# Optimization experiments

Measured on AMD Instinct MI355X. Metric: run time of the kernel, lower is better.

The kernel has to match this reference:

```python
import jax, jax.numpy as jnp
import numpy as np

HEADS = 16
D_MODEL = 1024
D_HEAD = D_MODEL // HEADS


def setup_inputs() -> dict:
    key = jax.random.key(0)
    ks = jax.random.split(key, 9)
    s_h = 1.0 / np.sqrt(D_HEAD)
    s_m = 1.0 / np.sqrt(D_MODEL)
    return {
        "x": jax.random.normal(ks[0], (4, 2048, D_MODEL), dtype=jnp.float32),
        "Wq": jax.random.uniform(ks[1], (D_HEAD, D_HEAD), jnp.float32, -s_h, s_h),
        "bq": jax.random.uniform(ks[2], (D_HEAD,), jnp.float32, -s_h, s_h),
        "Wk": jax.random.uniform(ks[3], (D_HEAD, D_HEAD), jnp.float32, -s_h, s_h),
        "bk": jax.random.uniform(ks[4], (D_HEAD,), jnp.float32, -s_h, s_h),
        "Wv": jax.random.uniform(ks[5], (D_HEAD, D_HEAD), jnp.float32, -s_h, s_h),
        "bv": jax.random.uniform(ks[6], (D_HEAD,), jnp.float32, -s_h, s_h),
        "Wp": jax.random.uniform(ks[7], (D_MODEL, D_MODEL), jnp.float32, -s_m, s_m),
        "bp": jax.random.uniform(ks[8], (D_MODEL,), jnp.float32, -s_m, s_m),
    }


def reference(x, Wq, bq, Wk, bk, Wv, bv, Wp, bp):
    B, T, C = x.shape
    xh = x.reshape(B, T, HEADS, D_HEAD)  # [B,T,H,Dh]
    # per-head linear projections (torch Linear: x @ W.T + b)
    q = jnp.einsum('bthd,ed->bhte', xh, Wq) + bq  # [B,H,T,Dh]
    k = jnp.einsum('bthd,ed->bhte', xh, Wk) + bk
    v = jnp.einsum('bthd,ed->bhte', xh, Wv) + bv
    # NOTE: original scales by sqrt(C) = sqrt(d_model), not sqrt(d_head)
    att = jnp.einsum('bhqd,bhkd->bhqk', q, k) / jnp.sqrt(jnp.float32(C))
    att = jax.nn.softmax(att, axis=-1)
    out = jnp.einsum('bhqk,bhkd->bhqd', att, v)  # [B,H,T,Dh]
    out = out.transpose(0, 2, 1, 3).reshape(B, T, C)
    return out @ Wp.T + bp
```

## Files before the change

### kernel.cpp

```cpp
#include <hip/hip_runtime.h>
#include <hip/hip_bf16.h>
#include <cstddef>

#define B_  4
#define T_  2048
#define H_  16
#define DH  64
#define C_  1024
#define BH  64

typedef float  f32x16 __attribute__((ext_vector_type(16)));
typedef __bf16 bf16x8 __attribute__((ext_vector_type(8)));
typedef __bf16 bf16x4 __attribute__((ext_vector_type(4)));

#define MFMA32(a, b, c) __builtin_amdgcn_mfma_f32_32x32x16_bf16(a, b, c, 0, 0, 0)


__device__ __forceinline__ unsigned cvt_pk_bf16(float lo, float hi) {
    unsigned r;
    asm("v_cvt_pk_bf16_f32 %0, %1, %2" : "=v"(r) : "v"(lo), "v"(hi));
    return r;
}

__global__ __launch_bounds__(256) void qkv_kernel(
    const float* __restrict__ x,
    const float* __restrict__ Wq, const float* __restrict__ bq,
    const float* __restrict__ Wk, const float* __restrict__ bk,
    const float* __restrict__ Wv, const float* __restrict__ bv,
    __bf16* __restrict__ q, __bf16* __restrict__ k, __bf16* __restrict__ vt)
{
    __shared__ __bf16 Xs[128 * 72];
    __shared__ __bf16 Ws[3][64 * 72];
    __bf16* Vtl = Xs;

    const int tt  = blockIdx.x;
    const int bh  = blockIdx.y;
    const int b   = bh >> 4, h = bh & 15;
    const int t0  = tt * 128;
    const int tid = threadIdx.x;
    const int wave = tid >> 6, lane = tid & 63;
    const int m = lane & 31, hh = lane >> 5;

    #pragma unroll
    for (int i = 0; i < 8; ++i) {
        const int idx = i * 256 + tid;
        const int r = idx >> 4, c = (idx & 15) * 4;
        const float4 x4 = *(const float4*)(x + ((size_t)(b * T_ + t0 + r)) * C_ + h * DH + c);
        const unsigned lo = ((unsigned)__builtin_bit_cast(unsigned short, (__bf16)x4.y) << 16)
                          | (unsigned)__builtin_bit_cast(unsigned short, (__bf16)x4.x);
        const unsigned hi = ((unsigned)__builtin_bit_cast(unsigned short, (__bf16)x4.w) << 16)
                          | (unsigned)__builtin_bit_cast(unsigned short, (__bf16)x4.z);
        *(unsigned*)&Xs[r * 72 + c]     = lo;
        *(unsigned*)&Xs[r * 72 + c + 2] = hi;
    }
    #pragma unroll
    for (int i = 0; i < 4; ++i) {
        const int idx = i * 256 + tid;
        const int r = idx >> 4, c = (idx & 15) * 4;
        const float* wsrc[3] = {Wq, Wk, Wv};
        #pragma unroll
        for (int wv_ = 0; wv_ < 3; ++wv_) {
            const float4 w4 = *(const float4*)(wsrc[wv_] + r * 64 + c);
            const unsigned lo = ((unsigned)__builtin_bit_cast(unsigned short, (__bf16)w4.y) << 16)
                              | (unsigned)__builtin_bit_cast(unsigned short, (__bf16)w4.x);
            const unsigned hi = ((unsigned)__builtin_bit_cast(unsigned short, (__bf16)w4.w) << 16)
                              | (unsigned)__builtin_bit_cast(unsigned short, (__bf16)w4.z);
            *(unsigned*)&Ws[wv_][r * 72 + c]     = lo;
            *(unsigned*)&Ws[wv_][r * 72 + c + 2] = hi;
        }
    }
    __syncthreads();

    bf16x8 xf[4];
    #pragma unroll
    for (int ks = 0; ks < 4; ++ks)
        xf[ks] = *(const bf16x8*)&Xs[(wave * 32 + m) * 72 + ks * 16 + hh * 8];
    __syncthreads();

    const float s32 = 0.03125f * 1.4426950408889634f;

    #pragma unroll
    for (int mat = 0; mat < 3; ++mat) {
        f32x16 acc0 = {}, acc1 = {};
        #pragma unroll
        for (int ks = 0; ks < 4; ++ks) {
            const bf16x8 w0 = *(const bf16x8*)&Ws[mat][(m) * 72 + ks * 16 + hh * 8];
            const bf16x8 w1 = *(const bf16x8*)&Ws[mat][(32 + m) * 72 + ks * 16 + hh * 8];
            acc0 = MFMA32(xf[ks], w0, acc0);
            acc1 = MFMA32(xf[ks], w1, acc1);
        }
        const float* bias = (mat == 0) ? bq : (mat == 1) ? bk : bv;
        const float b0 = bias[m], b1 = bias[32 + m];
        #pragma unroll
        for (int r = 0; r < 16; ++r) {
            const int R = (r & 3) + 8 * (r >> 2) + 4 * hh;
            const int tloc = wave * 32 + R;
            const float v0 = acc0[r] + b0, v1 = acc1[r] + b1;
            if (mat == 0) {
                const size_t base = ((size_t)bh * T_ + t0 + tloc) * DH;
                q[base + m]      = (__bf16)(v0 * s32);
                q[base + 32 + m] = (__bf16)(v1 * s32);
            } else if (mat == 1) {
                const size_t base = ((size_t)bh * T_ + t0 + tloc) * DH;
                k[base + m]      = (__bf16)v0;
                k[base + 32 + m] = (__bf16)v1;
            } else {
                Vtl[(m) * 136 + tloc]      = (__bf16)v0;
                Vtl[(32 + m) * 136 + tloc] = (__bf16)v1;
            }
        }
    }
    __syncthreads();
    #pragma unroll
    for (int i = 0; i < 4; ++i) {
        const int idx = i * 256 + tid;
        const int e = idx >> 4, c = (idx & 15) * 8;
        *(uint4*)(vt + ((size_t)(bh * 64 + e)) * T_ + t0 + c) = *(uint4*)&Vtl[e * 136 + c];
    }
}

__global__ __launch_bounds__(256, 2) void attn_kernel(
    const __bf16* __restrict__ q, const __bf16* __restrict__ k,
    const __bf16* __restrict__ vt, __bf16* __restrict__ o)
{
    __shared__ __bf16 smem[2][2][64 * 72];

    const int bh  = blockIdx.x;
    const int q0  = blockIdx.y * 256;
    const int tid = threadIdx.x;
    const int wave = tid >> 6, lane = tid & 63;
    const int m = lane & 31, h = lane >> 5;

    const __bf16* qb = q  + (size_t)bh * T_ * DH;
    const __bf16* kb = k  + (size_t)bh * T_ * DH;
    const __bf16* vb = vt + (size_t)bh * DH * T_;

    bf16x8 qf[2][4];
    #pragma unroll
    for (int hf = 0; hf < 2; ++hf)
        #pragma unroll
        for (int ks = 0; ks < 4; ++ks)
            qf[hf][ks] = *(const bf16x8*)(qb +
                (size_t)(q0 + wave * 64 + hf * 32 + m) * DH + ks * 16 + h * 8);

    const int r0s = tid >> 3;
    const int c0s = (tid & 7) * 8;

    uint4 kreg[2], vreg[2];
    #pragma unroll
    for (int i = 0; i < 2; ++i) {
        kreg[i] = *(const uint4*)(kb + (size_t)(r0s + 32 * i) * DH + c0s);
        vreg[i] = *(const uint4*)(vb + (size_t)(r0s + 32 * i) * T_ + c0s);
    }
    #pragma unroll
    for (int i = 0; i < 2; ++i) {
        *(uint4*)&smem[0][0][(r0s + 32 * i) * 72 + c0s] = kreg[i];
        *(uint4*)&smem[0][1][(r0s + 32 * i) * 72 + c0s] = vreg[i];
    }

    f32x16 O00 = {}, O01 = {}, O10 = {}, O11 = {};
    float ls0 = 0.f, ls1 = 0.f;

    int cur = 0;
    for (int kt = 0; kt < T_; kt += 64) {
        __syncthreads();
        const bool pre = (kt + 64 < T_);
        if (pre) {
            #pragma unroll
            for (int i = 0; i < 2; ++i) {
                kreg[i] = *(const uint4*)(kb + (size_t)(kt + 64 + r0s + 32 * i) * DH + c0s);
                vreg[i] = *(const uint4*)(vb + (size_t)(r0s + 32 * i) * T_ + kt + 64 + c0s);
            }
        }
        const __bf16* Ksb  = &smem[cur][0][0];
        const __bf16* Vtsb = &smem[cur][1][0];

        bf16x8 kf[2][4], vf[2][4];
        #pragma unroll
        for (int rh = 0; rh < 2; ++rh)
            #pragma unroll
            for (int ks = 0; ks < 4; ++ks)
                kf[rh][ks] = *(const bf16x8*)&Ksb[(rh * 32 + m) * 72 + ks * 16 + h * 8];
        #pragma unroll
        for (int dh = 0; dh < 2; ++dh)
            #pragma unroll
            for (int c = 0; c < 4; ++c)
                vf[dh][c] = *(const bf16x8*)&Vtsb[(dh * 32 + m) * 72 + c * 16 + h * 8];

        #pragma unroll
        for (int hf = 0; hf < 2; ++hf) {
            float lsum = 0.f;
            #pragma unroll
            for (int rh = 0; rh < 2; ++rh) {
                f32x16 S = {};
                #pragma unroll
                for (int ks = 0; ks < 4; ++ks)
                    S = MFMA32(kf[rh][ks], qf[hf][ks], S);

                #pragma unroll
                for (int cc = 0; cc < 2; ++cc) {
                    const int rb = cc * 8;
                    float e0 = __builtin_amdgcn_exp2f(S[rb + 0]);
                    float e1 = __builtin_amdgcn_exp2f(S[rb + 1]);
                    float e2 = __builtin_amdgcn_exp2f(S[rb + 2]);
                    float e3 = __builtin_amdgcn_exp2f(S[rb + 3]);
                    float e4 = __builtin_amdgcn_exp2f(S[rb + 4]);
                    float e5 = __builtin_amdgcn_exp2f(S[rb + 5]);
                    float e6 = __builtin_amdgcn_exp2f(S[rb + 6]);
                    float e7 = __builtin_amdgcn_exp2f(S[rb + 7]);
                    lsum += ((e0 + e1) + (e2 + e3)) + ((e4 + e5) + (e6 + e7));
                    unsigned a0 = cvt_pk_bf16(e0, e1);
                    unsigned a1 = cvt_pk_bf16(e2, e3);
                    unsigned b0 = cvt_pk_bf16(e4, e5);
                    unsigned b1 = cvt_pk_bf16(e6, e7);
                    asm("v_permlane32_swap_b32 %0, %1" : "+v"(a0), "+v"(b0));
                    asm("v_permlane32_swap_b32 %0, %1" : "+v"(a1), "+v"(b1));
                    const uint4 pw = {a0, a1, b0, b1};
                    const bf16x8 pb = __builtin_bit_cast(bf16x8, pw);
                    const int c = rh * 2 + cc;
                    if (hf == 0) {
                        O00 = MFMA32(vf[0][c], pb, O00);
                        O01 = MFMA32(vf[1][c], pb, O01);
                    } else {
                        O10 = MFMA32(vf[0][c], pb, O10);
                        O11 = MFMA32(vf[1][c], pb, O11);
                    }
                }
            }
            if (hf == 0) ls0 += lsum; else ls1 += lsum;
        }

        if (pre) {
            #pragma unroll
            for (int i = 0; i < 2; ++i) {
                *(uint4*)&smem[cur ^ 1][0][(r0s + 32 * i) * 72 + c0s] = kreg[i];
                *(uint4*)&smem[cur ^ 1][1][(r0s + 32 * i) * 72 + c0s] = vreg[i];
            }
        }
        cur ^= 1;
    }

    ls0 += __shfl_xor(ls0, 32);
    ls1 += __shfl_xor(ls1, 32);
    const float li0 = 1.0f / ls0, li1 = 1.0f / ls1;

    __syncthreads();
    __bf16* Os = &smem[0][0][0];

    #pragma unroll
    for (int g = 0; g < 4; ++g) {
        bf16x4 w00, w01, w10, w11;
        #pragma unroll
        for (int j = 0; j < 4; ++j) {
            w00[j] = (__bf16)(O00[4 * g + j] * li0);
            w01[j] = (__bf16)(O01[4 * g + j] * li0);
            w10[j] = (__bf16)(O10[4 * g + j] * li1);
            w11[j] = (__bf16)(O11[4 * g + j] * li1);
        }
        const int row0 = (wave * 64 + m) * 72;
        const int row1 = (wave * 64 + 32 + m) * 72;
        *(bf16x4*)&Os[row0 + 8 * g + 4 * h]      = w00;
        *(bf16x4*)&Os[row0 + 32 + 8 * g + 4 * h] = w01;
        *(bf16x4*)&Os[row1 + 8 * g + 4 * h]      = w10;
        *(bf16x4*)&Os[row1 + 32 + 8 * g + 4 * h] = w11;
    }
    __syncthreads();

    __bf16* ob = o + ((size_t)bh * T_ + q0) * DH;
    #pragma unroll
    for (int i = 0; i < 8; ++i) {
        const int idx = i * 256 + tid;
        const int r = idx >> 3, c = (idx & 7) * 8;
        *(uint4*)(ob + (size_t)r * DH + c) = *(uint4*)&Os[r * 72 + c];
    }
}

__global__ __launch_bounds__(256) void wpconv_kernel(
    const float* __restrict__ Wp, __bf16* __restrict__ Wpb)
{
    const size_t idx = (size_t)(blockIdx.x * 256 + threadIdx.x) * 4;
    const float4 w4 = *(const float4*)(Wp + idx);
    const unsigned lo = ((unsigned)__builtin_bit_cast(unsigned short, (__bf16)w4.y) << 16)
                      | (unsigned)__builtin_bit_cast(unsigned short, (__bf16)w4.x);
    const unsigned hi = ((unsigned)__builtin_bit_cast(unsigned short, (__bf16)w4.w) << 16)
                      | (unsigned)__builtin_bit_cast(unsigned short, (__bf16)w4.z);
    uint2 p; p.x = lo; p.y = hi;
    *(uint2*)(Wpb + idx) = p;
}

__global__ __launch_bounds__(256) void proj_kernel(
    const __bf16* __restrict__ a,
    const __bf16* __restrict__ Wpb, const float* __restrict__ bp,
    float* __restrict__ out)
{
    __shared__ __bf16 As[128 * 72];
    __shared__ __bf16 Bs[128 * 72];

    const int tb = blockIdx.x, eb = blockIdx.y;
    const int tid = threadIdx.x;
    const int wave = tid >> 6, lane = tid & 63;
    const int m = lane & 31, h = lane >> 5;
    const int tok0 = tb * 128;
    const int b = tok0 >> 11, t0 = tok0 & (T_ - 1);
    const int e0 = eb * 128;

    f32x16 acc[4] = {f32x16{}, f32x16{}, f32x16{}, f32x16{}};

    for (int cb = 0; cb < 16; ++cb) {
        __syncthreads();
        #pragma unroll
        for (int i = 0; i < 4; ++i) {
            const int idx = i * 256 + tid;
            const int r = idx >> 3, c = (idx & 7) * 8;
            *(uint4*)&As[r * 72 + c] =
                *(const uint4*)(a + ((size_t)(b * H_ + cb) * T_ + t0 + r) * DH + c);
        }
        #pragma unroll
        for (int i = 0; i < 4; ++i) {
            const int idx = i * 256 + tid;
            const int r = idx >> 3, c = (idx & 7) * 8;
            *(uint4*)&Bs[r * 72 + c] =
                *(const uint4*)(Wpb + (size_t)(e0 + r) * C_ + cb * 64 + c);
        }
        __syncthreads();

        #pragma unroll
        for (int ks = 0; ks < 4; ++ks) {
            const bf16x8 af = *(const bf16x8*)&As[(wave * 32 + m) * 72 + ks * 16 + h * 8];
            #pragma unroll
            for (int n = 0; n < 4; ++n) {
                const bf16x8 bf = *(const bf16x8*)&Bs[(n * 32 + m) * 72 + ks * 16 + h * 8];
                acc[n] = MFMA32(af, bf, acc[n]);
            }
        }
    }

    #pragma unroll
    for (int n = 0; n < 4; ++n) {
        const int e = e0 + n * 32 + m;
        const float bias = bp[e];
        #pragma unroll
        for (int r = 0; r < 16; ++r) {
            const int R = (r & 3) + 8 * (r >> 2) + 4 * h;
            out[(size_t)(tok0 + wave * 32 + R) * C_ + e] = acc[n][r] + bias;
        }
    }
}

extern "C" void kernel_launch(void* const* d_in, const int* in_sizes, int n_in,
                              void* d_out, int out_size, void* d_ws, size_t ws_size,
                              hipStream_t stream)
{
    const float* x  = (const float*)d_in[0];
    const float* Wq = (const float*)d_in[1];
    const float* bq = (const float*)d_in[2];
    const float* Wk = (const float*)d_in[3];
    const float* bk = (const float*)d_in[4];
    const float* Wv = (const float*)d_in[5];
    const float* bv = (const float*)d_in[6];
    const float* Wp = (const float*)d_in[7];
    const float* bp = (const float*)d_in[8];

    const size_t N = (size_t)BH * T_ * DH;
    __bf16* qws  = (__bf16*)d_ws;
    __bf16* kws  = qws + N;
    __bf16* vtws = kws + N;
    __bf16* ows  = vtws + N;
    __bf16* wpb  = qws;

    qkv_kernel<<<dim3(16, 64), 256, 0, stream>>>(
        x, Wq, bq, Wk, bk, Wv, bv, qws, kws, vtws);
    attn_kernel<<<dim3(64, 8), 256, 0, stream>>>(qws, kws, vtws, ows);
    wpconv_kernel<<<dim3(1024), 256, 0, stream>>>(Wp, wpb);
    proj_kernel<<<dim3(64, 8), 256, 0, stream>>>(ows, wpb, bp, (float*)d_out);
}
```

Baseline: 229.5 us.

## Load K/V fragments directly from global into registers, dropping LDS staging

Removes the shared-memory double buffer for K and V tiles in the attention kernel. Each wave now loads its MFMA fragments straight from global memory, prefetching the next K tile into registers through an A/B ping-pong. V fragments are loaded at the start of each tile. This eliminates the per-tile __syncthreads and the LDS store/load round trips, but each of the 4 waves now fetches the same K/V data separately, relying on L1/L2 to absorb the redundancy. The V loads are not prefetched ahead of use.

```diff
diff --git a/kernel.cpp b/kernel.cpp
--- a/kernel.cpp
+++ b/kernel.cpp
@@ -119,11 +119,75 @@
     }
 }
 
+__device__ __forceinline__ void attn_tile(
+    const __bf16* __restrict__ kb, const __bf16* __restrict__ vb,
+    int kt, int ktn,
+    const bf16x8 (&kcur)[2][4], bf16x8 (&knxt)[2][4],
+    const bf16x8 (&qf)[2][4],
+    f32x16& O00, f32x16& O01, f32x16& O10, f32x16& O11,
+    float& ls0, float& ls1, int m, int h)
+{
+    bf16x8 vf[2][4];
+    #pragma unroll
+    for (int dh = 0; dh < 2; ++dh)
+        #pragma unroll
+        for (int c = 0; c < 4; ++c)
+            vf[dh][c] = *(const bf16x8*)(vb + (size_t)(dh * 32 + m) * T_ + kt + c * 16 + h * 8);
+    #pragma unroll
+    for (int rh = 0; rh < 2; ++rh)
+        #pragma unroll
+        for (int ks = 0; ks < 4; ++ks)
+            knxt[rh][ks] = *(const bf16x8*)(kb + (size_t)(ktn + rh * 32 + m) * DH + ks * 16 + h * 8);
+
+    #pragma unroll
+    for (int hf = 0; hf < 2; ++hf) {
+        float lsum = 0.f;
+        #pragma unroll
+        for (int rh = 0; rh < 2; ++rh) {
+            f32x16 S = {};
+            #pragma unroll
+            for (int ks = 0; ks < 4; ++ks)
+                S = MFMA32(kcur[rh][ks], qf[hf][ks], S);
+
+            #pragma unroll
+            for (int cc = 0; cc < 2; ++cc) {
+                const int rb = cc * 8;
+                float e0 = __builtin_amdgcn_exp2f(S[rb + 0]);
+                float e1 = __builtin_amdgcn_exp2f(S[rb + 1]);
+                float e2 = __builtin_amdgcn_exp2f(S[rb + 2]);
+                float e3 = __builtin_amdgcn_exp2f(S[rb + 3]);
+                float e4 = __builtin_amdgcn_exp2f(S[rb + 4]);
+                float e5 = __builtin_amdgcn_exp2f(S[rb + 5]);
+                float e6 = __builtin_amdgcn_exp2f(S[rb + 6]);
+                float e7 = __builtin_amdgcn_exp2f(S[rb + 7]);
+                lsum += ((e0 + e1) + (e2 + e3)) + ((e4 + e5) + (e6 + e7));
+                unsigned a0 = cvt_pk_bf16(e0, e1);
+                unsigned a1 = cvt_pk_bf16(e2, e3);
+                unsigned b0 = cvt_pk_bf16(e4, e5);
+                unsigned b1 = cvt_pk_bf16(e6, e7);
+                asm("v_permlane32_swap_b32 %0, %1" : "+v"(a0), "+v"(b0));
+                asm("v_permlane32_swap_b32 %0, %1" : "+v"(a1), "+v"(b1));
+                const uint4 pw = {a0, a1, b0, b1};
+                const bf16x8 pb = __builtin_bit_cast(bf16x8, pw);
+                const int c = rh * 2 + cc;
+                if (hf == 0) {
+                    O00 = MFMA32(vf[0][c], pb, O00);
+                    O01 = MFMA32(vf[1][c], pb, O01);
+                } else {
+                    O10 = MFMA32(vf[0][c], pb, O10);
+                    O11 = MFMA32(vf[1][c], pb, O11);
+                }
+            }
+        }
+        if (hf == 0) ls0 += lsum; else ls1 += lsum;
+    }
+}
+
 __global__ __launch_bounds__(256, 2) void attn_kernel(
     const __bf16* __restrict__ q, const __bf16* __restrict__ k,
     const __bf16* __restrict__ vt, __bf16* __restrict__ o)
 {
-    __shared__ __bf16 smem[2][2][64 * 72];
+    __shared__ __bf16 Os[256 * 72];
 
     const int bh  = blockIdx.x;
     const int q0  = blockIdx.y * 256;
@@ -143,109 +207,26 @@
             qf[hf][ks] = *(const bf16x8*)(qb +
                 (size_t)(q0 + wave * 64 + hf * 32 + m) * DH + ks * 16 + h * 8);
 
-    const int r0s = tid >> 3;
-    const int c0s = (tid & 7) * 8;
-
-    uint4 kreg[2], vreg[2];
-    #pragma unroll
-    for (int i = 0; i < 2; ++i) {
-        kreg[i] = *(const uint4*)(kb + (size_t)(r0s + 32 * i) * DH + c0s);
-        vreg[i] = *(const uint4*)(vb + (size_t)(r0s + 32 * i) * T_ + c0s);
-    }
-    #pragma unroll
-    for (int i = 0; i < 2; ++i) {
-        *(uint4*)&smem[0][0][(r0s + 32 * i) * 72 + c0s] = kreg[i];
-        *(uint4*)&smem[0][1][(r0s + 32 * i) * 72 + c0s] = vreg[i];
-    }
-
     f32x16 O00 = {}, O01 = {}, O10 = {}, O11 = {};
     float ls0 = 0.f, ls1 = 0.f;
 
-    int cur = 0;
-    for (int kt = 0; kt < T_; kt += 64) {
-        __syncthreads();
-        const bool pre = (kt + 64 < T_);
-        if (pre) {
-            #pragma unroll
-            for (int i = 0; i < 2; ++i) {
-                kreg[i] = *(const uint4*)(kb + (size_t)(kt + 64 + r0s + 32 * i) * DH + c0s);
-                vreg[i] = *(const uint4*)(vb + (size_t)(r0s + 32 * i) * T_ + kt + 64 + c0s);
-            }
-        }
-        const __bf16* Ksb  = &smem[cur][0][0];
-        const __bf16* Vtsb = &smem[cur][1][0];
-
-        bf16x8 kf[2][4], vf[2][4];
-        #pragma unroll
-        for (int rh = 0; rh < 2; ++rh)
-            #pragma unroll
-            for (int ks = 0; ks < 4; ++ks)
-                kf[rh][ks] = *(const bf16x8*)&Ksb[(rh * 32 + m) * 72 + ks * 16 + h * 8];
-        #pragma unroll
-        for (int dh = 0; dh < 2; ++dh)
-            #pragma unroll
-            for (int c = 0; c < 4; ++c)
-                vf[dh][c] = *(const bf16x8*)&Vtsb[(dh * 32 + m) * 72 + c * 16 + h * 8];
-
-        #pragma unroll
-        for (int hf = 0; hf < 2; ++hf) {
-            float lsum = 0.f;
-            #pragma unroll
-            for (int rh = 0; rh < 2; ++rh) {
-                f32x16 S = {};
-                #pragma unroll
-                for (int ks = 0; ks < 4; ++ks)
-                    S = MFMA32(kf[rh][ks], qf[hf][ks], S);
-
-                #pragma unroll
-                for (int cc = 0; cc < 2; ++cc) {
-                    const int rb = cc * 8;
-                    float e0 = __builtin_amdgcn_exp2f(S[rb + 0]);
-                    float e1 = __builtin_amdgcn_exp2f(S[rb + 1]);
-                    float e2 = __builtin_amdgcn_exp2f(S[rb + 2]);
-                    float e3 = __builtin_amdgcn_exp2f(S[rb + 3]);
-                    float e4 = __builtin_amdgcn_exp2f(S[rb + 4]);
-                    float e5 = __builtin_amdgcn_exp2f(S[rb + 5]);
-                    float e6 = __builtin_amdgcn_exp2f(S[rb + 6]);
-                    float e7 = __builtin_amdgcn_exp2f(S[rb + 7]);
-                    lsum += ((e0 + e1) + (e2 + e3)) + ((e4 + e5) + (e6 + e7));
-                    unsigned a0 = cvt_pk_bf16(e0, e1);
-                    unsigned a1 = cvt_pk_bf16(e2, e3);
-                    unsigned b0 = cvt_pk_bf16(e4, e5);
-                    unsigned b1 = cvt_pk_bf16(e6, e7);
-                    asm("v_permlane32_swap_b32 %0, %1" : "+v"(a0), "+v"(b0));
-                    asm("v_permlane32_swap_b32 %0, %1" : "+v"(a1), "+v"(b1));
-                    const uint4 pw = {a0, a1, b0, b1};
-                    const bf16x8 pb = __builtin_bit_cast(bf16x8, pw);
-                    const int c = rh * 2 + cc;
-                    if (hf == 0) {
-                        O00 = MFMA32(vf[0][c], pb, O00);
-                        O01 = MFMA32(vf[1][c], pb, O01);
-                    } else {
-                        O10 = MFMA32(vf[0][c], pb, O10);
-                        O11 = MFMA32(vf[1][c], pb, O11);
-                    }
-                }
-            }
-            if (hf == 0) ls0 += lsum; else ls1 += lsum;
-        }
-
-        if (pre) {
-            #pragma unroll
-            for (int i = 0; i < 2; ++i) {
-                *(uint4*)&smem[cur ^ 1][0][(r0s + 32 * i) * 72 + c0s] = kreg[i];
-                *(uint4*)&smem[cur ^ 1][1][(r0s + 32 * i) * 72 + c0s] = vreg[i];
-            }
-        }
-        cur ^= 1;
+    bf16x8 kfA[2][4], kfB[2][4];
+    #pragma unroll
+    for (int rh = 0; rh < 2; ++rh)
+        #pragma unroll
+        for (int ks = 0; ks < 4; ++ks)
+            kfA[rh][ks] = *(const bf16x8*)(kb + (size_t)(rh * 32 + m) * DH + ks * 16 + h * 8);
+
+    for (int kt = 0; kt < T_; kt += 128) {
+        attn_tile(kb, vb, kt,      kt + 64,              kfA, kfB, qf,
+                  O00, O01, O10, O11, ls0, ls1, m, h);
+        attn_tile(kb, vb, kt + 64, (kt + 128) & (T_ - 1), kfB, kfA, qf,
+                  O00, O01, O10, O11, ls0, ls1, m, h);
     }
 
     ls0 += __shfl_xor(ls0, 32);
     ls1 += __shfl_xor(ls1, 32);
     const float li0 = 1.0f / ls0, li1 = 1.0f / ls1;
-
-    __syncthreads();
-    __bf16* Os = &smem[0][0][0];
 
     #pragma unroll
     for (int g = 0; g < 4; ++g) {
```

Measured after the change: 271.7 us. 1.18x slower.
